# Optimization experiments

Measured on AMD Instinct MI355X. Metric: run time of the kernel, lower is better.

Reference implementation:

```python
import jax, jax.numpy as jnp
import numpy as np

B, L, H, D_IN = 64, 4096, 128, 3

def setup_inputs() -> dict:
    key = jax.random.key(0)
    ks = jax.random.split(key, 9)
    def lin_w(k, fan_in, shape):
        bound = 1.0 / np.sqrt(fan_in)
        return jax.random.uniform(k, shape, jnp.float32, -bound, bound)
    return {
        "x": jax.random.normal(ks[0], (B, L, D_IN), jnp.float32),
        "Wp": lin_w(ks[1], D_IN, (D_IN, H)), "bp": lin_w(ks[2], D_IN, (H,)),
        "Wz": lin_w(ks[3], H, (H, H)),      "bz": lin_w(ks[4], H, (H,)),
        "Wh": lin_w(ks[5], H, (H, H)),      "bh": lin_w(ks[6], H, (H,)),
        "Wg": lin_w(ks[7], H, (H, 1)),      "bg": lin_w(ks[8], H, (1,)),
    }

def reference(x, Wp, bp, Wz, bz, Wh, bh, Wg, bg):
    # Batched projections across all timesteps (B, L, H)
    inp = x @ Wp + bp                      # input_proj
    z = jax.nn.sigmoid(inp @ Wz + bz)      # update gate
    h_tilde = jnp.tanh(inp @ Wh + bh)      # candidate
    # Linear recurrence h_t = a_t * h_{t-1} + b_t, h_{-1} = 0
    a = 1.0 - z
    b = z * h_tilde
    def combine(c1, c2):
        a1, b1 = c1
        a2, b2 = c2
        return (a1 * a2, b1 * a2 + b2)
    _, h = jax.lax.associative_scan(combine, (a, b), axis=1)  # h_t (since h_{-1}=0)
    # Readout uses h BEFORE the update at each step: preds_t = gauss_head(h_{t-1})
    h_prev = jnp.concatenate([jnp.zeros_like(h[:, :1]), h[:, :-1]], axis=1)
    preds = h_prev @ Wg + bg               # (B, L, 1)
    return preds
```

## Files before the change

kernel.cpp:

```cpp
#include <hip/hip_runtime.h>
#include <hip/hip_bf16.h>
#include <stdint.h>

#define B_   64
#define L_   4096
#define H_   128
#define T_   64
#define C_   (L_/T_)
#define BH_  (B_*H_)
#define PADI 136
#define PWS  72

typedef __attribute__((ext_vector_type(8))) short short8;
typedef __attribute__((ext_vector_type(4))) short short4v;
typedef __attribute__((ext_vector_type(4))) float floatx4;

#define LOG2E 1.44269504088896340736f

__device__ __forceinline__ unsigned short f2bf(float f){
    unsigned int u = __float_as_uint(f);
    u += 0x7FFFu + ((u >> 16) & 1u);
    return (unsigned short)(u >> 16);
}
__device__ __forceinline__ float bf2f(unsigned short s){
    return __uint_as_float(((unsigned int)s) << 16);
}

__global__ void prep_w(const float* __restrict__ Wz, const float* __restrict__ Wh,
                       unsigned short* __restrict__ WzT, unsigned short* __restrict__ WhT){
    int b = blockIdx.x;
    const float* W = (b < 16) ? Wz : Wh;
    unsigned short* WT = (b < 16) ? WzT : WhT;
    int b16 = b & 15, tid = threadIdx.x;
    #pragma unroll
    for (int it = 0; it < 4; ++it){
        int idx = b16*1024 + it*256 + tid;
        int n = idx >> 7, k = idx & 127;
        WT[idx] = f2bf(W[k*H_ + n]);
    }
}


__global__ __launch_bounds__(256, 3)
void gates_agg(const float* __restrict__ x,
               const float* __restrict__ Wp, const float* __restrict__ bp,
               const float* __restrict__ bz, const float* __restrict__ bh,
               const float* __restrict__ Wg,
               const unsigned short* __restrict__ WzT,
               const unsigned short* __restrict__ WhT,
               float* __restrict__ aggA, float* __restrict__ aggH,
               float* __restrict__ sloc, unsigned short* __restrict__ pw_g)
{
    __shared__ __align__(16) unsigned short s_ab[H_*H_];
    __shared__ __align__(16) unsigned short s_pw[H_*PWS];
    __shared__ float s_bz[H_], s_bh[H_], s_wg[H_];
    unsigned short* inp_lds = s_ab;

    const int bid = blockIdx.x;
    const int bb  = bid / C_;
    const int cc  = bid % C_;
    const int t0g = cc * T_;
    const int tid = threadIdx.x;
    const int wv = tid >> 6, lane = tid & 63, quad = lane >> 4, l15 = lane & 15;

    if (tid < H_){ s_bz[tid] = bz[tid]; s_bh[tid] = bh[tid]; s_wg[tid] = Wg[tid]; }

    #pragma unroll
    for (int it = 0; it < 4; ++it){
        int idx = tid + it*256;
        int t = idx >> 4, h0 = (idx & 15) * 8;
        const float* xr = x + ((size_t)bb*L_ + t0g + t)*3;
        float x0 = xr[0], x1 = xr[1], x2 = xr[2];
        short8 pk;
        #pragma unroll
        for (int m = 0; m < 8; ++m){
            int hh = h0 + m;
            float v = bp[hh];
            v = fmaf(x0, Wp[hh],      v);
            v = fmaf(x1, Wp[H_+hh],   v);
            v = fmaf(x2, Wp[2*H_+hh], v);
            pk[m] = (short)f2bf(v);
        }
        *(short8*)&inp_lds[t*PADI + h0] = pk;
    }
    __syncthreads();

    const int ct0 = wv*2;

    floatx4 accz[4][2];
    #pragma unroll
    for (int r = 0; r < 4; ++r)
        #pragma unroll
        for (int c = 0; c < 2; ++c) accz[r][c] = (floatx4){0.f,0.f,0.f,0.f};
    #pragma unroll
    for (int kk = 0; kk < 4; ++kk){
        short8 af[4], bfr[2];
        #pragma unroll
        for (int r = 0; r < 4; ++r)
            af[r] = *(const short8*)&inp_lds[(r*16 + l15)*PADI + kk*32 + quad*8];
        #pragma unroll
        for (int c = 0; c < 2; ++c)
            bfr[c] = *(const short8*)&WzT[((ct0+c)*16 + l15)*H_ + kk*32 + quad*8];
        #pragma unroll
        for (int r = 0; r < 4; ++r)
            #pragma unroll
            for (int c = 0; c < 2; ++c)
                accz[r][c] = __builtin_amdgcn_mfma_f32_16x16x32_bf16(af[r], bfr[c], accz[r][c], 0, 0, 0);
    }

    unsigned int a2[4][2][2];
    #pragma unroll
    for (int r = 0; r < 4; ++r){
        #pragma unroll
        for (int c = 0; c < 2; ++c){
            int col = (ct0+c)*16 + l15;
            float vbz = s_bz[col];
            unsigned short q[4];
            #pragma unroll
            for (int e = 0; e < 4; ++e){
                float szb = accz[r][c][e] + vbz;
                float a = __builtin_amdgcn_rcpf(1.0f + __builtin_amdgcn_exp2f(szb * LOG2E));
                q[e] = f2bf(a);
            }
            a2[r][c][0] = (unsigned int)q[0] | ((unsigned int)q[1] << 16);
            a2[r][c][1] = (unsigned int)q[2] | ((unsigned int)q[3] << 16);
        }
    }

    floatx4 acch[4][2];
    #pragma unroll
    for (int r = 0; r < 4; ++r)
        #pragma unroll
        for (int c = 0; c < 2; ++c) acch[r][c] = (floatx4){0.f,0.f,0.f,0.f};
    #pragma unroll
    for (int kk = 0; kk < 4; ++kk){
        short8 af[4], bfr[2];
        #pragma unroll
        for (int r = 0; r < 4; ++r)
            af[r] = *(const short8*)&inp_lds[(r*16 + l15)*PADI + kk*32 + quad*8];
        #pragma unroll
        for (int c = 0; c < 2; ++c)
            bfr[c] = *(const short8*)&WhT[((ct0+c)*16 + l15)*H_ + kk*32 + quad*8];
        #pragma unroll
        for (int r = 0; r < 4; ++r)
            #pragma unroll
            for (int c = 0; c < 2; ++c)
                acch[r][c] = __builtin_amdgcn_mfma_f32_16x16x32_bf16(af[r], bfr[c], acch[r][c], 0, 0, 0);
    }
    __syncthreads();

    #pragma unroll
    for (int r = 0; r < 4; ++r){
        #pragma unroll
        for (int c = 0; c < 2; ++c){
            int col = (ct0+c)*16 + l15;
            float vbh = s_bh[col];
            short8 pk;
            #pragma unroll
            for (int e = 0; e < 4; ++e){
                unsigned short abf = (unsigned short)(a2[r][c][e>>1] >> ((e & 1)*16));
                float a = bf2f(abf);
                float z = 1.0f - a;
                float shb = acch[r][c][e] + vbh;
                float e2 = __builtin_amdgcn_exp2f(2.0f*LOG2E*fabsf(shb));
                float tt = 1.0f - 2.0f*__builtin_amdgcn_rcpf(e2 + 1.0f);
                float bt = z * copysignf(tt, shb);
                pk[2*e]   = (short)abf;
                pk[2*e+1] = (short)f2bf(bt);
            }
            int ch = (r*4 + quad) ^ l15;
            *(short8*)&s_ab[col*H_ + ch*8] = pk;
        }
    }
    __syncthreads();

    if (tid < H_){
        float A = 1.0f, h = 0.0f;
        float wgv = s_wg[tid];
        #pragma unroll
        for (int t4 = 0; t4 < 16; ++t4){
            int base = tid*H_ + ((t4 ^ (tid & 15)) << 3);
            short8 pr = *(const short8*)&s_ab[base];
            short4v pw4;
            #pragma unroll
            for (int e = 0; e < 4; ++e){
                float aa = bf2f((unsigned short)pr[2*e]);
                float bv = bf2f((unsigned short)pr[2*e+1]);
                s_ab[base + 2*e] = f2bf(h * wgv);
                pw4[e] = (short)f2bf(A * wgv);
                A *= aa;
                h = fmaf(aa, h, bv);
            }
            *(short4v*)&s_pw[tid*PWS + t4*4] = pw4;
        }
        aggA[cc*BH_ + bb*H_ + tid] = A;
        aggH[cc*BH_ + bb*H_ + tid] = h;
    }
    __syncthreads();

    {
        int t = tid >> 2, q = tid & 3;
        float s = 0.0f;
        #pragma unroll
        for (int j = 0; j < 32; ++j){
            int col = q*32 + j;
            s += bf2f(s_ab[col*H_ + (((t >> 2) ^ (col & 15)) << 3) + (t & 3)*2]);
        }
        s += __shfl_xor(s, 1, 64);
        s += __shfl_xor(s, 2, 64);
        if (q == 0) sloc[(size_t)bid*T_ + t] = s;
    }

    {
        unsigned short* dst = pw_g + (size_t)bid * (H_*PWS);
        #pragma unroll
        for (int i = 0; i < 4; ++i){
            int idx = tid + i*256;
            *(short8*)&dst[idx*8] = *(const short8*)&s_pw[idx*8];
        }
        if (tid < 128){
            int idx = 1024 + tid;
            *(short8*)&dst[idx*8] = *(const short8*)&s_pw[idx*8];
        }
    }
}

__global__ __launch_bounds__(256, 4)
void apply2(const unsigned short* __restrict__ pw_g,
            const float* __restrict__ aggA, const float* __restrict__ aggH,
            const float* __restrict__ sloc, const float* __restrict__ bg,
            float* __restrict__ preds)
{
    __shared__ float s_u[H_*65];
    const int bid = blockIdx.x;
    const int bb  = bid / C_;
    const int cc  = bid % C_;
    const int t0g = cc * T_;
    const int tid = threadIdx.x;

    if (tid < H_){
        float cval = 0.0f;
        #pragma unroll
        for (int ch = 0; ch < C_; ++ch){
            float ga = aggA[ch*BH_ + bb*H_ + tid];
            float gh = aggH[ch*BH_ + bb*H_ + tid];
            bool in = ch < cc;
            cval = fmaf(in ? ga : 1.0f, cval, in ? gh : 0.0f);
        }
        const unsigned short* row = pw_g + (size_t)bid*(H_*PWS) + tid*PWS;
        #pragma unroll
        for (int i = 0; i < 8; ++i){
            short8 pw8 = *(const short8*)&row[i*8];
            #pragma unroll
            for (int e = 0; e < 8; ++e)
                s_u[tid*65 + i*8 + e] = cval * bf2f((unsigned short)pw8[e]);
        }
    }
    __syncthreads();

    int t = tid >> 2, q = tid & 3;
    float s = 0.0f;
    #pragma unroll
    for (int j = 0; j < 32; ++j){
        int col = q*32 + j;
        s += s_u[col*65 + t];
    }
    s += __shfl_xor(s, 1, 64);
    s += __shfl_xor(s, 2, 64);
    if (q == 0)
        preds[(size_t)bb*L_ + t0g + t] = s + sloc[(size_t)bid*T_ + t] + bg[0];
}

extern "C" void kernel_launch(void* const* d_in, const int* in_sizes, int n_in,
                              void* d_out, int out_size, void* d_ws, size_t ws_size,
                              hipStream_t stream){
    const float* x  = (const float*)d_in[0];
    const float* Wp = (const float*)d_in[1];
    const float* bp = (const float*)d_in[2];
    const float* Wz = (const float*)d_in[3];
    const float* bz = (const float*)d_in[4];
    const float* Wh = (const float*)d_in[5];
    const float* bh = (const float*)d_in[6];
    const float* Wg = (const float*)d_in[7];
    const float* bg = (const float*)d_in[8];
    float* preds = (float*)d_out;

    uint8_t* w8 = (uint8_t*)d_ws;
    unsigned short* WzT = (unsigned short*)(w8);
    unsigned short* WhT = (unsigned short*)(w8 + 32768);
    float* aggA = (float*)(w8 + 65536);
    float* aggH = (float*)(w8 + 65536 + 4u*BH_*C_);
    float* sloc = (float*)(w8 + 65536 + 8u*BH_*C_);
    unsigned short* pw_g = (unsigned short*)(w8 + 65536 + 12u*BH_*C_);

    hipLaunchKernelGGL(prep_w, dim3(32), dim3(256), 0, stream, Wz, Wh, WzT, WhT);
    hipLaunchKernelGGL(gates_agg, dim3(B_*C_), dim3(256), 0, stream,
                       x, Wp, bp, bz, bh, Wg, WzT, WhT, aggA, aggH, sloc, pw_g);
    hipLaunchKernelGGL(apply2, dim3(B_*C_), dim3(256), 0, stream,
                       pw_g, aggA, aggH, sloc, bg, preds);
}
```

Baseline: 171.9 us.

## Drop s_pw LDS staging, write pw directly, and async-load pw in apply

```diff
diff --git a/kernel.cpp b/kernel.cpp
--- a/kernel.cpp
+++ b/kernel.cpp
@@ -9,7 +9,6 @@
 #define C_   (L_/T_)
 #define BH_  (B_*H_)
 #define PADI 136
-#define PWS  72
 
 typedef __attribute__((ext_vector_type(8))) short short8;
 typedef __attribute__((ext_vector_type(4))) short short4v;
@@ -41,7 +40,7 @@
 }
 
 
-__global__ __launch_bounds__(256, 3)
+__global__ __launch_bounds__(256, 4)
 void gates_agg(const float* __restrict__ x,
                const float* __restrict__ Wp, const float* __restrict__ bp,
                const float* __restrict__ bz, const float* __restrict__ bh,
@@ -52,8 +51,8 @@
                float* __restrict__ sloc, unsigned short* __restrict__ pw_g)
 {
     __shared__ __align__(16) unsigned short s_ab[H_*H_];
-    __shared__ __align__(16) unsigned short s_pw[H_*PWS];
     __shared__ float s_bz[H_], s_bh[H_], s_wg[H_];
+    __shared__ float s_part[256];
     unsigned short* inp_lds = s_ab;
 
     const int bid = blockIdx.x;
@@ -108,59 +107,42 @@
                 accz[r][c] = __builtin_amdgcn_mfma_f32_16x16x32_bf16(af[r], bfr[c], accz[r][c], 0, 0, 0);
     }
 
-    unsigned int a2[4][2][2];
+    floatx4 acch[4][2];
+    #pragma unroll
+    for (int r = 0; r < 4; ++r)
+        #pragma unroll
+        for (int c = 0; c < 2; ++c) acch[r][c] = (floatx4){0.f,0.f,0.f,0.f};
+    #pragma unroll
+    for (int kk = 0; kk < 4; ++kk){
+        short8 af[4], bfr[2];
+        #pragma unroll
+        for (int r = 0; r < 4; ++r)
+            af[r] = *(const short8*)&inp_lds[(r*16 + l15)*PADI + kk*32 + quad*8];
+        #pragma unroll
+        for (int c = 0; c < 2; ++c)
+            bfr[c] = *(const short8*)&WhT[((ct0+c)*16 + l15)*H_ + kk*32 + quad*8];
+        #pragma unroll
+        for (int r = 0; r < 4; ++r)
+            #pragma unroll
+            for (int c = 0; c < 2; ++c)
+                acch[r][c] = __builtin_amdgcn_mfma_f32_16x16x32_bf16(af[r], bfr[c], acch[r][c], 0, 0, 0);
+    }
+    __syncthreads();
+
     #pragma unroll
     for (int r = 0; r < 4; ++r){
         #pragma unroll
         for (int c = 0; c < 2; ++c){
             int col = (ct0+c)*16 + l15;
-            float vbz = s_bz[col];
-            unsigned short q[4];
+            float vbz = s_bz[col], vbh = s_bh[col];
+            short8 pk;
             #pragma unroll
             for (int e = 0; e < 4; ++e){
                 float szb = accz[r][c][e] + vbz;
                 float a = __builtin_amdgcn_rcpf(1.0f + __builtin_amdgcn_exp2f(szb * LOG2E));
-                q[e] = f2bf(a);
-            }
-            a2[r][c][0] = (unsigned int)q[0] | ((unsigned int)q[1] << 16);
-            a2[r][c][1] = (unsigned int)q[2] | ((unsigned int)q[3] << 16);
-        }
-    }
-
-    floatx4 acch[4][2];
-    #pragma unroll
-    for (int r = 0; r < 4; ++r)
-        #pragma unroll
-        for (int c = 0; c < 2; ++c) acch[r][c] = (floatx4){0.f,0.f,0.f,0.f};
-    #pragma unroll
-    for (int kk = 0; kk < 4; ++kk){
-        short8 af[4], bfr[2];
-        #pragma unroll
-        for (int r = 0; r < 4; ++r)
-            af[r] = *(const short8*)&inp_lds[(r*16 + l15)*PADI + kk*32 + quad*8];
-        #pragma unroll
-        for (int c = 0; c < 2; ++c)
-            bfr[c] = *(const short8*)&WhT[((ct0+c)*16 + l15)*H_ + kk*32 + quad*8];
-        #pragma unroll
-        for (int r = 0; r < 4; ++r)
-            #pragma unroll
-            for (int c = 0; c < 2; ++c)
-                acch[r][c] = __builtin_amdgcn_mfma_f32_16x16x32_bf16(af[r], bfr[c], acch[r][c], 0, 0, 0);
-    }
-    __syncthreads();
-
-    #pragma unroll
-    for (int r = 0; r < 4; ++r){
-        #pragma unroll
-        for (int c = 0; c < 2; ++c){
-            int col = (ct0+c)*16 + l15;
-            float vbh = s_bh[col];
-            short8 pk;
-            #pragma unroll
-            for (int e = 0; e < 4; ++e){
-                unsigned short abf = (unsigned short)(a2[r][c][e>>1] >> ((e & 1)*16));
-                float a = bf2f(abf);
-                float z = 1.0f - a;
+                unsigned short abf = f2bf(a);
+                float af_ = bf2f(abf);
+                float z = 1.0f - af_;
                 float shb = acch[r][c][e] + vbh;
                 float e2 = __builtin_amdgcn_exp2f(2.0f*LOG2E*fabsf(shb));
                 float tt = 1.0f - 2.0f*__builtin_amdgcn_rcpf(e2 + 1.0f);
@@ -177,21 +159,27 @@
     if (tid < H_){
         float A = 1.0f, h = 0.0f;
         float wgv = s_wg[tid];
+        unsigned short* pwdst = pw_g + (size_t)bid*(T_*H_) + tid*T_;
         #pragma unroll
         for (int t4 = 0; t4 < 16; ++t4){
             int base = tid*H_ + ((t4 ^ (tid & 15)) << 3);
             short8 pr = *(const short8*)&s_ab[base];
-            short4v pw4;
+            short8 wb;
+            short4v pq;
             #pragma unroll
             for (int e = 0; e < 4; ++e){
                 float aa = bf2f((unsigned short)pr[2*e]);
                 float bv = bf2f((unsigned short)pr[2*e+1]);
-                s_ab[base + 2*e] = f2bf(h * wgv);
-                pw4[e] = (short)f2bf(A * wgv);
+                unsigned short hwq = f2bf(h * wgv);
+                unsigned short pwq = f2bf(A * wgv);
+                wb[2*e]   = (short)hwq;
+                wb[2*e+1] = (short)pwq;
+                pq[e]     = (short)pwq;
                 A *= aa;
                 h = fmaf(aa, h, bv);
             }
-            *(short4v*)&s_pw[tid*PWS + t4*4] = pw4;
+            *(short8*)&s_ab[base] = wb;
+            *(short4v*)&pwdst[t4*4] = pq;
         }
         aggA[cc*BH_ + bb*H_ + tid] = A;
         aggH[cc*BH_ + bb*H_ + tid] = h;
@@ -199,30 +187,20 @@
     __syncthreads();
 
     {
-        int t = tid >> 2, q = tid & 3;
+        int t = tid & 63, w4 = tid >> 6;
+        int t4 = t >> 2, e2 = (t & 3)*2;
         float s = 0.0f;
         #pragma unroll
         for (int j = 0; j < 32; ++j){
-            int col = q*32 + j;
-            s += bf2f(s_ab[col*H_ + (((t >> 2) ^ (col & 15)) << 3) + (t & 3)*2]);
-        }
-        s += __shfl_xor(s, 1, 64);
-        s += __shfl_xor(s, 2, 64);
-        if (q == 0) sloc[(size_t)bid*T_ + t] = s;
-    }
-
-    {
-        unsigned short* dst = pw_g + (size_t)bid * (H_*PWS);
-        #pragma unroll
-        for (int i = 0; i < 4; ++i){
-            int idx = tid + i*256;
-            *(short8*)&dst[idx*8] = *(const short8*)&s_pw[idx*8];
-        }
-        if (tid < 128){
-            int idx = 1024 + tid;
-            *(short8*)&dst[idx*8] = *(const short8*)&s_pw[idx*8];
-        }
-    }
+            int col = w4*32 + j;
+            s += bf2f(s_ab[col*H_ + ((t4 ^ (col & 15)) << 3) + e2]);
+        }
+        s_part[w4*64 + t] = s;
+    }
+    __syncthreads();
+    if (tid < 64)
+        sloc[(size_t)bid*T_ + tid] =
+            s_part[tid] + s_part[64+tid] + s_part[128+tid] + s_part[192+tid];
 }
 
 __global__ __launch_bounds__(256, 4)
@@ -231,13 +209,27 @@
             const float* __restrict__ sloc, const float* __restrict__ bg,
             float* __restrict__ preds)
 {
-    __shared__ float s_u[H_*65];
+    __shared__ __align__(16) unsigned short s_pw[T_*H_];
+    __shared__ float s_c[H_];
+    __shared__ float s_part[256];
     const int bid = blockIdx.x;
     const int bb  = bid / C_;
     const int cc  = bid % C_;
     const int t0g = cc * T_;
     const int tid = threadIdx.x;
-
+    const int wv = tid >> 6, lane = tid & 63;
+
+    {
+        const char* src = (const char*)(pw_g + (size_t)bid*(T_*H_));
+        char* dst = (char*)s_pw;
+        #pragma unroll
+        for (int i = 0; i < 4; ++i){
+            int off = (wv*4 + i)*1024;
+            __builtin_amdgcn_global_load_lds(
+                (const __attribute__((address_space(1))) unsigned int*)(src + off + lane*16),
+                (__attribute__((address_space(3))) unsigned int*)(dst + off), 16, 0, 0);
+        }
+    }
     if (tid < H_){
         float cval = 0.0f;
         #pragma unroll
@@ -247,28 +239,25 @@
             bool in = ch < cc;
             cval = fmaf(in ? ga : 1.0f, cval, in ? gh : 0.0f);
         }
-        const unsigned short* row = pw_g + (size_t)bid*(H_*PWS) + tid*PWS;
-        #pragma unroll
-        for (int i = 0; i < 8; ++i){
-            short8 pw8 = *(const short8*)&row[i*8];
-            #pragma unroll
-            for (int e = 0; e < 8; ++e)
-                s_u[tid*65 + i*8 + e] = cval * bf2f((unsigned short)pw8[e]);
-        }
-    }
-    __syncthreads();
-
-    int t = tid >> 2, q = tid & 3;
-    float s = 0.0f;
-    #pragma unroll
-    for (int j = 0; j < 32; ++j){
-        int col = q*32 + j;
-        s += s_u[col*65 + t];
-    }
-    s += __shfl_xor(s, 1, 64);
-    s += __shfl_xor(s, 2, 64);
-    if (q == 0)
-        preds[(size_t)bb*L_ + t0g + t] = s + sloc[(size_t)bid*T_ + t] + bg[0];
+        s_c[tid] = cval;
+    }
+    __syncthreads();
+
+    {
+        int t = tid & 63, w4 = tid >> 6;
+        float s = 0.0f;
+        #pragma unroll
+        for (int j = 0; j < 32; ++j){
+            int col = w4*32 + j;
+            s += s_c[col] * bf2f(s_pw[col*T_ + t]);
+        }
+        s_part[w4*64 + t] = s;
+    }
+    __syncthreads();
+    if (tid < 64){
+        float s = s_part[tid] + s_part[64+tid] + s_part[128+tid] + s_part[192+tid];
+        preds[(size_t)bb*L_ + t0g + tid] = s + sloc[(size_t)bid*T_ + tid] + bg[0];
+    }
 }
 
 extern "C" void kernel_launch(void* const* d_in, const int* in_sizes, int n_in,
```

New measurement: 160.9 us. 6.4% less time.
